# Kernel optimization log

Hardware: AMD Instinct MI355X
Metric: run time of the kernel (lower is better)

## Reference

```python
import jax, jax.numpy as jnp
import numpy as np

B, T = 128, 24
E = 512      # word_emb_size (== img feature dim)
H = 512      # hidden_size
V = 12000    # vocab_size


def setup_inputs() -> dict:
    key = jax.random.key(0)
    ks = jax.random.split(key, 8)
    s_e = 1.0 / np.sqrt(E)
    s_h = 1.0 / np.sqrt(H)
    return {
        "img": jax.random.normal(ks[0], (B, E), dtype=jnp.float32),
        "cap": jax.random.randint(ks[1], (B, T), 0, V, dtype=jnp.int64),
        "caplen": jax.random.randint(ks[2], (B,), 1, T + 1, dtype=jnp.int64),
        "emb": jax.random.normal(ks[3], (V, E), dtype=jnp.float32),
        "W_ih": jax.random.uniform(ks[4], (3 * H, E), jnp.float32, -s_h, s_h),
        "W_hh": jax.random.uniform(ks[5], (3 * H, H), jnp.float32, -s_h, s_h),
        "b_ih": jnp.zeros((3 * H,), jnp.float32),
        "b_hh": jnp.zeros((3 * H,), jnp.float32),
        "W_out": jax.random.uniform(ks[6], (V, H), jnp.float32, -s_h, s_h),
        "b_out": jax.random.uniform(ks[7], (V,), jnp.float32, -s_h, s_h),
    }


def _gru_decode(img, cap, emb, W_ih, W_hh, b_ih, b_hh, W_out, b_out):
    word_emb = emb[cap]                                   # [B, T, E]
    x_cat = jnp.concatenate([img[:, None, :], word_emb[:, :-1, :]], axis=1)  # [B, T, E]
    # Precompute input-gate projections for all steps (one big GEMM).
    gx = jnp.einsum('bte,ge->btg', x_cat, W_ih) + b_ih    # [B, T, 3H]
    h0 = jnp.zeros((img.shape[0], H), x_cat.dtype)

    def step(h, gx_t):
        gh = h @ W_hh.T + b_hh                            # [B, 3H]
        xr, xz, xn = jnp.split(gx_t, 3, axis=-1)
        hr, hz, hn = jnp.split(gh, 3, axis=-1)
        r = jax.nn.sigmoid(xr + hr)
        z = jax.nn.sigmoid(xz + hz)
        n = jnp.tanh(xn + r * hn)
        h_new = (1.0 - z) * n + z * h
        return h_new, h_new

    _, hs = jax.lax.scan(step, h0, jnp.swapaxes(gx, 0, 1))  # hs: [T, B, H]
    logits = jnp.einsum('tbh,vh->btv', hs, W_out) + b_out   # [B, T, V]
    return logits


def reference(img, cap, caplen, emb, W_ih, W_hh, b_ih, b_hh, W_out, b_out):
    # caplen only sets the (static here) unroll length in the original loop.
    predictions = _gru_decode(img, cap, emb, W_ih, W_hh, b_ih, b_hh, W_out, b_out)
    return predictions
```

## Files before the change

kernel.cpp:

```cpp
#include <hip/hip_runtime.h>
#include <hip/hip_bf16.h>
#include <cstdint>
#include <cstddef>

typedef __bf16 bf16;
typedef __bf16 bf16x8 __attribute__((ext_vector_type(8)));
typedef __bf16 bf16x4 __attribute__((ext_vector_type(4)));
typedef float  f32x4  __attribute__((ext_vector_type(4)));

#define TT 24
#define BB 128
#define EE 512
#define HH 512
#define VV 12000
#define VPAD 12032
#define THREEH 1536
#define MTOT (TT*BB)
#define NBLK 32

#define GLDS(gp, lp)                                                              \
  __builtin_amdgcn_global_load_lds(                                               \
      (const __attribute__((address_space(1))) void*)(const void*)(gp),           \
      (__attribute__((address_space(3))) void*)(void*)(lp), 16, 0, 0)
#define GLDS_COH(gp, lp)                                                          \
  __builtin_amdgcn_global_load_lds(                                               \
      (const __attribute__((address_space(1))) void*)(const void*)(gp),           \
      (__attribute__((address_space(3))) void*)(void*)(lp), 16, 0, 17)

#define QX   (MTOT*EE/4)
#define QIH  (THREEH*EE/4)
#define QHH  (THREEH*HH/4)
#define QOUT (VPAD*HH/4)
#define QTOT (QX+QIH+QHH+QOUT)

__global__ __launch_bounds__(256) void prep(const float* __restrict__ img,
                                            const int* __restrict__ cap,
                                            const float* __restrict__ emb,
                                            const float* __restrict__ W_ih,
                                            const float* __restrict__ W_hh,
                                            const float* __restrict__ W_out,
                                            bf16* __restrict__ X,
                                            bf16* __restrict__ Wih_b,
                                            bf16* __restrict__ Whh_b,
                                            bf16* __restrict__ Wout_b) {
  int q = blockIdx.x * 256 + threadIdx.x;
  if (q < QX) {
    int m = q >> 7, e4 = q & 127;
    int t = m >> 7, b = m & 127;
    const float* src;
    if (t == 0) src = img + (size_t)b * EE;
    else        src = emb + (size_t)cap[b * TT + (t - 1)] * EE;
    float4 v = *(const float4*)(src + e4 * 4);
    bf16x4 o = { (bf16)v.x, (bf16)v.y, (bf16)v.z, (bf16)v.w };
    *(bf16x4*)(X + (size_t)m * EE + e4 * 4) = o;
    return;
  }
  q -= QX;
  if (q < QIH) {
    float4 v = *(const float4*)(W_ih + (size_t)q * 4);
    bf16x4 o = { (bf16)v.x, (bf16)v.y, (bf16)v.z, (bf16)v.w };
    *(bf16x4*)(Wih_b + (size_t)q * 4) = o;
    return;
  }
  q -= QIH;
  if (q < QHH) {
    float4 v = *(const float4*)(W_hh + (size_t)q * 4);
    bf16x4 o = { (bf16)v.x, (bf16)v.y, (bf16)v.z, (bf16)v.w };
    *(bf16x4*)(Whh_b + (size_t)q * 4) = o;
    return;
  }
  q -= QHH;
  if (q < QOUT) {
    size_t i = (size_t)q * 4;
    float4 v = make_float4(0.f, 0.f, 0.f, 0.f);
    if (i + 4 <= (size_t)VV * HH) v = *(const float4*)(W_out + i);
    bf16x4 o = { (bf16)v.x, (bf16)v.y, (bf16)v.z, (bf16)v.w };
    *(bf16x4*)(Wout_b + i) = o;
  }
}

template <int PERM>
__global__ __launch_bounds__(256) void gemm_bt(const bf16* __restrict__ A,
                                               const bf16* __restrict__ Bm,
                                               const float* __restrict__ bias,
                                               float* __restrict__ C,
                                               int N, int Nvalid) {
  const int K = 512;
  __shared__ __align__(16) bf16 Alds[128 * 32];
  __shared__ __align__(16) bf16 Blds[128 * 32];
  const int tid  = threadIdx.x;
  const int lane = tid & 63;
  const int wv   = tid >> 6;
  const int wr   = wv >> 1, wc = wv & 1;
  const int m0 = blockIdx.y * 128, n0 = blockIdx.x * 128;
  const bf16* Ab = A + (size_t)m0 * K;
  const bf16* Bb = Bm + (size_t)n0 * K;
  const int srow = tid >> 2;
  const int skq  = (tid & 3) * 8;

  f32x4 acc[4][4];
#pragma unroll
  for (int i = 0; i < 4; i++)
#pragma unroll
    for (int j = 0; j < 4; j++) acc[i][j] = 0.f;

  for (int kt = 0; kt < K; kt += 32) {
    __syncthreads();
    GLDS(Ab + (size_t)srow * K + kt + skq,        Alds + srow * 32 + skq);
    GLDS(Ab + (size_t)(srow + 64) * K + kt + skq, Alds + (srow + 64) * 32 + skq);
    GLDS(Bb + (size_t)srow * K + kt + skq,        Blds + srow * 32 + skq);
    GLDS(Bb + (size_t)(srow + 64) * K + kt + skq, Blds + (srow + 64) * 32 + skq);
    asm volatile("s_waitcnt vmcnt(0)" ::: "memory");
    __syncthreads();

    const int fr = lane & 15, kh = lane >> 4;
    bf16x8 af[4], bfv[4];
#pragma unroll
    for (int i = 0; i < 4; i++)
      af[i] = *(const bf16x8*)(Alds + (wr * 64 + i * 16 + fr) * 32 + kh * 8);
#pragma unroll
    for (int j = 0; j < 4; j++)
      bfv[j] = *(const bf16x8*)(Blds + (wc * 64 + j * 16 + fr) * 32 + kh * 8);
#pragma unroll
    for (int i = 0; i < 4; i++)
#pragma unroll
      for (int j = 0; j < 4; j++)
        acc[i][j] = __builtin_amdgcn_mfma_f32_16x16x32_bf16(af[i], bfv[j], acc[i][j], 0, 0, 0);
  }

  const int fr = lane & 15, fq = lane >> 4;
#pragma unroll
  for (int j = 0; j < 4; j++) {
    int n = n0 + wc * 64 + j * 16 + fr;
    if (n >= Nvalid) continue;
    float bv = bias ? bias[n] : 0.f;
#pragma unroll
    for (int i = 0; i < 4; i++) {
#pragma unroll
      for (int r = 0; r < 4; r++) {
        int m = m0 + wr * 64 + i * 16 + fq * 4 + r;
        float v = acc[i][j][r] + bv;
        size_t off;
        if (PERM) off = (size_t)(m & 127) * (TT * (size_t)VV) + (size_t)(m >> 7) * VV + n;
        else      off = (size_t)m * N + n;
        C[off] = v;
      }
    }
  }
}

__global__ __launch_bounds__(256) void gru_all(unsigned* __restrict__ HswA,
                                               unsigned* __restrict__ HswB,
                                               const bf16* __restrict__ Whh_b,
                                               const float* __restrict__ gx,
                                               const float* __restrict__ b_hh,
                                               bf16* __restrict__ hs,
                                               unsigned* __restrict__ barcnt) {
  __shared__ __align__(16) bf16 Wlds[48 * 512];
  __shared__ __align__(16) bf16 Alds[4][2][32 * 128];

  const int tid  = threadIdx.x;
  const int lane = tid & 63;
  const int wv   = tid >> 6;
  const int j0   = blockIdx.x * 16;
  const int fr   = lane & 15;
  const int kh   = lane >> 4;
  const int j    = j0 + fr;

#pragma unroll
  for (int i = 0; i < 12; ++i) {
    int r  = i * 4 + wv;
    int g  = r >> 4, jj = r & 15;
    bf16x8 v = *(const bf16x8*)(Whh_b + (size_t)(g * HH + j0 + jj) * 512 + lane * 8);
    int dst = r * 1024 + ((lane * 16) ^ ((r & 7) << 4));
    *(bf16x8*)((char*)Wlds + dst) = v;
  }
  __syncthreads();

  const float bh0 = b_hh[j], bh1 = b_hh[HH + j], bh2 = b_hh[2 * HH + j];

  float hreg[2][4];
#pragma unroll
  for (int mi = 0; mi < 2; mi++)
#pragma unroll
    for (int r = 0; r < 4; r++) hreg[mi][r] = 0.f;

  auto stageA = [&](const unsigned* hin, int kc, int buf) {
    const bf16* hb = (const bf16*)hin;
#pragma unroll
    for (int i = 0; i < 8; ++i) {
      int rr = i * 4 + kh;
      int cc = fr * 8;
      int src = (wv * 32 + rr) * 512 + kc * 128 + (cc ^ ((rr & 7) << 3));
      GLDS_COH(hb + src, &Alds[wv][buf][0] + rr * 128 + cc);
    }
  };

  for (int t = 0; t < TT; ++t) {
    float pxr[2][4], pxz[2][4], pxn[2][4];
#pragma unroll
    for (int mi = 0; mi < 2; mi++)
#pragma unroll
      for (int r = 0; r < 4; r++) {
        int bb = wv * 32 + mi * 16 + kh * 4 + r;
        const float* gb = gx + (size_t)(t * BB + bb) * THREEH + j;
        pxr[mi][r] = gb[0];
        pxz[mi][r] = gb[512];
        pxn[mi][r] = gb[1024];
      }

    f32x4 acc[2][3];
#pragma unroll
    for (int mi = 0; mi < 2; mi++)
#pragma unroll
      for (int g = 0; g < 3; g++) acc[mi][g] = 0.f;

    if (t > 0) {
      const unsigned* hi = (t & 1) ? HswA : HswB;
      stageA(hi, 0, 0);
#pragma unroll
      for (int kc = 0; kc < 4; ++kc) {
        const int buf = kc & 1;
        if (kc < 3) {
          stageA(hi, kc + 1, buf ^ 1);
          asm volatile("s_waitcnt vmcnt(8)" ::: "memory");
        } else {
          asm volatile("s_waitcnt vmcnt(0)" ::: "memory");
        }
#pragma unroll
        for (int kk = 0; kk < 4; ++kk) {
          bf16x8 af[2], bfv[3];
#pragma unroll
          for (int mi = 0; mi < 2; mi++)
            af[mi] = *(const bf16x8*)((char*)&Alds[wv][buf][0] +
                       (mi * 16 + fr) * 256 + ((kk * 64 + kh * 16) ^ ((fr & 7) << 4)));
#pragma unroll
          for (int g = 0; g < 3; g++)
            bfv[g] = *(const bf16x8*)((char*)Wlds + (g * 16 + fr) * 1024 +
                       ((kc * 256 + kk * 64 + kh * 16) ^ ((fr & 7) << 4)));
#pragma unroll
          for (int mi = 0; mi < 2; mi++)
#pragma unroll
            for (int g = 0; g < 3; g++)
              acc[mi][g] = __builtin_amdgcn_mfma_f32_16x16x32_bf16(af[mi], bfv[g], acc[mi][g], 0, 0, 0);
        }
      }
    }

    unsigned* ho = (t & 1) ? HswB : HswA;
    unsigned* hs32 = (unsigned*)hs;
#pragma unroll
    for (int mi = 0; mi < 2; mi++) {
#pragma unroll
      for (int r = 0; r < 4; r++) {
        int bb  = wv * 32 + mi * 16 + kh * 4 + r;
        int row = t * BB + bb;
        float hr = acc[mi][0][r] + bh0;
        float hz = acc[mi][1][r] + bh1;
        float hn = acc[mi][2][r] + bh2;
        float rg = 1.f / (1.f + __expf(-(pxr[mi][r] + hr)));
        float zg = 1.f / (1.f + __expf(-(pxz[mi][r] + hz)));
        float ng = tanhf(pxn[mi][r] + rg * hn);
        float hnew = (1.f - zg) * ng + zg * hreg[mi][r];
        hreg[mi][r] = hnew;
        unsigned mine  = (unsigned)__builtin_bit_cast(unsigned short, (bf16)hnew);
        unsigned other = (unsigned)__shfl_xor((int)mine, 1);
        if (!(lane & 1)) {
          unsigned word = mine | (other << 16);
          int elem = bb * 512 + j;
          __hip_atomic_store(&ho[elem >> 1], word, __ATOMIC_RELAXED, __HIP_MEMORY_SCOPE_AGENT);
          hs32[((size_t)row * 512 + j) >> 1] = word;
        }
      }
    }

    if (t < TT - 1) {
      __syncthreads();
      if (tid == 0) {
        __hip_atomic_fetch_add(barcnt, 1u, __ATOMIC_RELAXED, __HIP_MEMORY_SCOPE_AGENT);
        unsigned tgt = (unsigned)NBLK * (unsigned)(t + 1);
        while (__hip_atomic_load(barcnt, __ATOMIC_RELAXED, __HIP_MEMORY_SCOPE_AGENT) < tgt)
          __builtin_amdgcn_s_sleep(2);
      }
      __syncthreads();
    }
  }
}

extern "C" void kernel_launch(void* const* d_in, const int* in_sizes, int n_in,
                              void* d_out, int out_size, void* d_ws, size_t ws_size,
                              hipStream_t stream) {
  const float* img   = (const float*)d_in[0];
  const int*   cap   = (const int*)d_in[1];
  const float* emb   = (const float*)d_in[3];
  const float* W_ih  = (const float*)d_in[4];
  const float* W_hh  = (const float*)d_in[5];
  const float* b_ih  = (const float*)d_in[6];
  const float* b_hh  = (const float*)d_in[7];
  const float* W_out = (const float*)d_in[8];
  const float* b_out = (const float*)d_in[9];
  float* out = (float*)d_out;

  char* ws = (char*)d_ws;
  size_t off = 0;
  auto alloc = [&](size_t bytes) {
    void* p = ws + off;
    off = (off + bytes + 255) & ~(size_t)255;
    return p;
  };
  bf16*  X      = (bf16*)alloc((size_t)MTOT * EE * 2);
  bf16*  Wih_b  = (bf16*)alloc((size_t)THREEH * EE * 2);
  bf16*  Whh_b  = (bf16*)alloc((size_t)THREEH * HH * 2);
  bf16*  Wout_b = (bf16*)alloc((size_t)VPAD * HH * 2);
  float* gx     = (float*)alloc((size_t)MTOT * THREEH * 4);
  bf16*  hs     = (bf16*)alloc((size_t)MTOT * HH * 2);
  unsigned* HswA = (unsigned*)alloc((size_t)BB * HH * 2);
  unsigned* HswB = (unsigned*)alloc((size_t)BB * HH * 2);
  unsigned* barcnt = (unsigned*)alloc(256);

  hipMemsetAsync(barcnt, 0, 256, stream);

  prep<<<dim3((QTOT + 255) / 256), dim3(256), 0, stream>>>(
      img, cap, emb, W_ih, W_hh, W_out, X, Wih_b, Whh_b, Wout_b);

  gemm_bt<0><<<dim3(THREEH / 128, MTOT / 128), dim3(256), 0, stream>>>(
      X, Wih_b, b_ih, gx, THREEH, THREEH);

  gru_all<<<dim3(NBLK), dim3(256), 0, stream>>>(HswA, HswB, Whh_b, gx, b_hh, hs, barcnt);

  gemm_bt<1><<<dim3(VPAD / 128, MTOT / 128), dim3(256), 0, stream>>>(
      hs, Wout_b, b_out, out, VV, VV);
}
```

Baseline: 431.2 us.

## Use per-block step flags, triple-buffer hidden-state staging, prefetch gx, swizzle GEMM tiles

Each block in the persistent GRU kernel now sets its own per-step flag, and one wave polls all 32 flags, replacing the single shared atomic counter barrier. The next step's gx values are prefetched while waiting on that barrier. Hidden-state staging moves from two LDS buffers to three so more chunks of h are in flight at once. The GEMM kernels also remap workgroup ids into groups of eight to improve cache locality. These changes target barrier latency and load stalls on the serial recurrence, at the cost of more LDS and more code complexity.

```diff
diff --git a/kernel.cpp b/kernel.cpp
--- a/kernel.cpp
+++ b/kernel.cpp
@@ -92,7 +92,14 @@
   const int lane = tid & 63;
   const int wv   = tid >> 6;
   const int wr   = wv >> 1, wc = wv & 1;
-  const int m0 = blockIdx.y * 128, n0 = blockIdx.x * 128;
+
+  const int nwg = gridDim.x * gridDim.y;
+  const int wid = blockIdx.y * gridDim.x + blockIdx.x;
+  const int cpx = nwg >> 3;
+  const int swz = (wid & 7) * cpx + (wid >> 3);
+  const int bx = swz % gridDim.x, by = swz / gridDim.x;
+
+  const int m0 = by * 128, n0 = bx * 128;
   const bf16* Ab = A + (size_t)m0 * K;
   const bf16* Bb = Bm + (size_t)n0 * K;
   const int srow = tid >> 2;
@@ -155,9 +162,9 @@
                                                const float* __restrict__ gx,
                                                const float* __restrict__ b_hh,
                                                bf16* __restrict__ hs,
-                                               unsigned* __restrict__ barcnt) {
+                                               unsigned* __restrict__ flags) {
   __shared__ __align__(16) bf16 Wlds[48 * 512];
-  __shared__ __align__(16) bf16 Alds[4][2][32 * 128];
+  __shared__ __align__(16) bf16 Alds[4][3][32 * 128];
 
   const int tid  = threadIdx.x;
   const int lane = tid & 63;
@@ -196,8 +203,29 @@
     }
   };
 
-  for (int t = 0; t < TT; ++t) {
-    float pxr[2][4], pxz[2][4], pxn[2][4];
+  f32x4 acc[2][3];
+  auto computeKC = [&](int kc, int buf) {
+#pragma unroll
+    for (int kk = 0; kk < 4; ++kk) {
+      bf16x8 af[2], bfv[3];
+#pragma unroll
+      for (int mi = 0; mi < 2; mi++)
+        af[mi] = *(const bf16x8*)((char*)&Alds[wv][buf][0] +
+                   (mi * 16 + fr) * 256 + ((kk * 64 + kh * 16) ^ ((fr & 7) << 4)));
+#pragma unroll
+      for (int g = 0; g < 3; g++)
+        bfv[g] = *(const bf16x8*)((char*)Wlds + (g * 16 + fr) * 1024 +
+                   ((kc * 256 + kk * 64 + kh * 16) ^ ((fr & 7) << 4)));
+#pragma unroll
+      for (int mi = 0; mi < 2; mi++)
+#pragma unroll
+        for (int g = 0; g < 3; g++)
+          acc[mi][g] = __builtin_amdgcn_mfma_f32_16x16x32_bf16(af[mi], bfv[g], acc[mi][g], 0, 0, 0);
+    }
+  };
+
+  float pxr[2][4], pxz[2][4], pxn[2][4];
+  auto prefetchGX = [&](int t) {
 #pragma unroll
     for (int mi = 0; mi < 2; mi++)
 #pragma unroll
@@ -208,8 +236,10 @@
         pxz[mi][r] = gb[512];
         pxn[mi][r] = gb[1024];
       }
-
-    f32x4 acc[2][3];
+  };
+  prefetchGX(0);
+
+  for (int t = 0; t < TT; ++t) {
 #pragma unroll
     for (int mi = 0; mi < 2; mi++)
 #pragma unroll
@@ -218,33 +248,19 @@
     if (t > 0) {
       const unsigned* hi = (t & 1) ? HswA : HswB;
       stageA(hi, 0, 0);
-#pragma unroll
-      for (int kc = 0; kc < 4; ++kc) {
-        const int buf = kc & 1;
-        if (kc < 3) {
-          stageA(hi, kc + 1, buf ^ 1);
-          asm volatile("s_waitcnt vmcnt(8)" ::: "memory");
-        } else {
-          asm volatile("s_waitcnt vmcnt(0)" ::: "memory");
-        }
-#pragma unroll
-        for (int kk = 0; kk < 4; ++kk) {
-          bf16x8 af[2], bfv[3];
-#pragma unroll
-          for (int mi = 0; mi < 2; mi++)
-            af[mi] = *(const bf16x8*)((char*)&Alds[wv][buf][0] +
-                       (mi * 16 + fr) * 256 + ((kk * 64 + kh * 16) ^ ((fr & 7) << 4)));
-#pragma unroll
-          for (int g = 0; g < 3; g++)
-            bfv[g] = *(const bf16x8*)((char*)Wlds + (g * 16 + fr) * 1024 +
-                       ((kc * 256 + kk * 64 + kh * 16) ^ ((fr & 7) << 4)));
-#pragma unroll
-          for (int mi = 0; mi < 2; mi++)
-#pragma unroll
-            for (int g = 0; g < 3; g++)
-              acc[mi][g] = __builtin_amdgcn_mfma_f32_16x16x32_bf16(af[mi], bfv[g], acc[mi][g], 0, 0, 0);
-        }
-      }
+      stageA(hi, 1, 1);
+      stageA(hi, 2, 2);
+      asm volatile("s_waitcnt vmcnt(16)" ::: "memory");
+      computeKC(0, 0);
+      asm volatile("s_waitcnt lgkmcnt(0)" ::: "memory");
+      __builtin_amdgcn_sched_barrier(0);
+      stageA(hi, 3, 0);
+      asm volatile("s_waitcnt vmcnt(16)" ::: "memory");
+      computeKC(1, 1);
+      asm volatile("s_waitcnt vmcnt(8)" ::: "memory");
+      computeKC(2, 2);
+      asm volatile("s_waitcnt vmcnt(0)" ::: "memory");
+      computeKC(3, 0);
     }
 
     unsigned* ho = (t & 1) ? HswB : HswA;
@@ -276,11 +292,14 @@
 
     if (t < TT - 1) {
       __syncthreads();
-      if (tid == 0) {
-        __hip_atomic_fetch_add(barcnt, 1u, __ATOMIC_RELAXED, __HIP_MEMORY_SCOPE_AGENT);
-        unsigned tgt = (unsigned)NBLK * (unsigned)(t + 1);
-        while (__hip_atomic_load(barcnt, __ATOMIC_RELAXED, __HIP_MEMORY_SCOPE_AGENT) < tgt)
-          __builtin_amdgcn_s_sleep(2);
+      if (tid == 0)
+        __hip_atomic_store(&flags[(t * NBLK + blockIdx.x) * 4], 1u,
+                           __ATOMIC_RELAXED, __HIP_MEMORY_SCOPE_AGENT);
+      prefetchGX(t + 1);
+      if (wv == 0 && lane < NBLK) {
+        while (__hip_atomic_load(&flags[(t * NBLK + lane) * 4],
+                                 __ATOMIC_RELAXED, __HIP_MEMORY_SCOPE_AGENT) == 0)
+          __builtin_amdgcn_s_sleep(1);
       }
       __syncthreads();
     }
@@ -316,9 +335,9 @@
   bf16*  hs     = (bf16*)alloc((size_t)MTOT * HH * 2);
   unsigned* HswA = (unsigned*)alloc((size_t)BB * HH * 2);
   unsigned* HswB = (unsigned*)alloc((size_t)BB * HH * 2);
-  unsigned* barcnt = (unsigned*)alloc(256);
-
-  hipMemsetAsync(barcnt, 0, 256, stream);
+  unsigned* flags = (unsigned*)alloc((size_t)TT * NBLK * 16);
+
+  hipMemsetAsync(flags, 0, (size_t)TT * NBLK * 16, stream);
 
   prep<<<dim3((QTOT + 255) / 256), dim3(256), 0, stream>>>(
       img, cap, emb, W_ih, W_hh, W_out, X, Wih_b, Whh_b, Wout_b);
@@ -326,7 +345,7 @@
   gemm_bt<0><<<dim3(THREEH / 128, MTOT / 128), dim3(256), 0, stream>>>(
       X, Wih_b, b_ih, gx, THREEH, THREEH);
 
-  gru_all<<<dim3(NBLK), dim3(256), 0, stream>>>(HswA, HswB, Whh_b, gx, b_hh, hs, barcnt);
+  gru_all<<<dim3(NBLK), dim3(256), 0, stream>>>(HswA, HswB, Whh_b, gx, b_hh, hs, flags);
 
   gemm_bt<1><<<dim3(VPAD / 128, MTOT / 128), dim3(256), 0, stream>>>(
       hs, Wout_b, b_out, out, VV, VV);
```

Measured after the change: 425.4 us. Within noise of the previous version (-1.3%).
